# Optimization experiments

Hardware: AMD Instinct MI355X
Metric: run time of the kernel (lower is better)

## Reference

```python
import jax, jax.numpy as jnp
import numpy as np

DIN = 256
HID = 512

def setup_inputs() -> dict:
    key = jax.random.key(0)
    ks = jax.random.split(key, 9)
    s_in = 1.0 / np.sqrt(DIN)
    s_h = 1.0 / np.sqrt(HID)
    h = jax.random.normal(ks[0], (32, 1024, DIN), dtype=jnp.float32)
    Wv = jax.random.uniform(ks[1], (HID, DIN), jnp.float32, -s_in, s_in)
    bv = jax.random.uniform(ks[2], (HID,), jnp.float32, -s_in, s_in)
    Wk = jax.random.uniform(ks[3], (HID, DIN), jnp.float32, -s_in, s_in)
    bk = jax.random.uniform(ks[4], (HID,), jnp.float32, -s_in, s_in)
    Wq = jax.random.uniform(ks[5], (HID, DIN), jnp.float32, -s_in, s_in)
    bq = jax.random.uniform(ks[6], (HID,), jnp.float32, -s_in, s_in)
    Wo = jax.random.uniform(ks[7], (DIN, HID), jnp.float32, -s_h, s_h)
    bo = jax.random.uniform(ks[8], (DIN,), jnp.float32, -s_h, s_h)
    return {"h": h, "Wv": Wv, "bv": bv, "Wk": Wk, "bk": bk, "Wq": Wq, "bq": bq, "Wo": Wo, "bo": bo}

def reference(h, Wv, bv, Wk, bk, Wq, bq, Wo, bo):
    # relu-activated Q/K/V projections: [B, N, HID]
    v = jax.nn.relu(jnp.einsum('bnd,hd->bnh', h, Wv) + bv)
    q = jax.nn.relu(jnp.einsum('bnd,hd->bnh', h, Wq) + bq)
    k = jax.nn.relu(jnp.einsum('bnd,hd->bnh', h, Wk) + bk)
    # unscaled attention: [B, N, N]
    att = jax.nn.softmax(jnp.einsum('bnh,bmh->bnm', q, k), axis=2)
    out = jnp.einsum('bnm,bmh->bnh', att, v)          # [B, N, HID]
    out = jax.nn.relu(jnp.einsum('bnh,dh->bnd', out, Wo) + bo)  # [B, N, DIN]
    return out
```

## Files before the change

### kernel.cpp

```cpp
#include <hip/hip_runtime.h>
#include <cstdint>
#include <cstddef>

#define NB    32
#define SEQ   1024
#define DIN   256
#define HID   512
#define MTOT  32768

typedef _Float16 half_t;
typedef _Float16 half8  __attribute__((ext_vector_type(8)));
typedef _Float16 half4v __attribute__((ext_vector_type(4)));
typedef float    f32x4  __attribute__((ext_vector_type(4)));

typedef __attribute__((address_space(1))) const void* gas_ptr;
typedef __attribute__((address_space(3))) void*       las_ptr;

__global__ void cvt_kernel(const float* __restrict__ src, half_t* __restrict__ dst, int n4) {
    int i = blockIdx.x * blockDim.x + threadIdx.x;
    if (i < n4) {
        f32x4 v = ((const f32x4*)src)[i];
        half4v h;
        h[0] = (half_t)v[0]; h[1] = (half_t)v[1]; h[2] = (half_t)v[2]; h[3] = (half_t)v[3];
        ((half4v*)dst)[i] = h;
    }
}

__global__ void cvt4_kernel(const float* __restrict__ s0, const float* __restrict__ s1,
                            const float* __restrict__ s2, const float* __restrict__ s3,
                            half_t* __restrict__ d0, half_t* __restrict__ d1,
                            half_t* __restrict__ d2, half_t* __restrict__ d3, int n4) {
    int y = blockIdx.y;
    const float* s = y == 0 ? s0 : y == 1 ? s1 : y == 2 ? s2 : s3;
    half_t*      d = y == 0 ? d0 : y == 1 ? d1 : y == 2 ? d2 : d3;
    int i = blockIdx.x * blockDim.x + threadIdx.x;
    if (i < n4) {
        f32x4 v = ((const f32x4*)s)[i];
        half4v h;
        h[0] = (half_t)v[0]; h[1] = (half_t)v[1]; h[2] = (half_t)v[2]; h[3] = (half_t)v[3];
        ((half4v*)d)[i] = h;
    }
}

__global__ void pack_bias(const float* __restrict__ bv, const float* __restrict__ bk,
                          const float* __restrict__ bq, float* __restrict__ dst) {
    int t = threadIdx.x;
    if (t < HID) {
        dst[t]         = bv[t];
        dst[HID + t]   = bk[t];
        dst[2*HID + t] = bq[t];
    }
}

template<int MODE>
__global__ __launch_bounds__(256, 2) void gemm_k(
    const half_t* __restrict__ A, long lda, long a_bs,
    const half_t* __restrict__ Bw, long ldb, long b_bs,
    void* __restrict__ Out, long ldo, long o_bs,
    const float* __restrict__ bias,
    int Kdim, half_t* __restrict__ out2)
{
    __shared__ alignas(16) half_t As[128 * 32];
    __shared__ alignas(16) half_t Bs[128 * 32];

    const int t    = threadIdx.x;
    const int lane = t & 63;
    const int wave = t >> 6;
    const int wm   = wave >> 1;
    const int wn   = wave & 1;
    const int lanen = lane & 15;
    const int quad  = lane >> 4;
    const int z     = blockIdx.z;
    const long m0 = (long)blockIdx.x * 128;
    const long n0 = (long)blockIdx.y * 128;

    const half_t* Ab = A  + (long)z * a_bs;
    const half_t* Bb = Bw + (long)z * b_bs;

    f32x4 acc[4][4];
#pragma unroll
    for (int i = 0; i < 4; i++)
#pragma unroll
        for (int j = 0; j < 4; j++)
            acc[i][j] = f32x4{0.f, 0.f, 0.f, 0.f};

    const int c0 = t, c1 = t + 256;
    const int r0 = c0 >> 2, kc0 = c0 & 3;
    const int r1 = c1 >> 2, kc1 = c1 & 3;

    const half_t* gA0 = Ab + (m0 + r0) * lda + kc0 * 8;
    const half_t* gA1 = Ab + (m0 + r1) * lda + kc1 * 8;
    const half_t* gB0 = Bb + (n0 + r0) * ldb + kc0 * 8;
    const half_t* gB1 = Bb + (n0 + r1) * ldb + kc1 * 8;
    half_t* lA0 = &As[c0 * 8];
    half_t* lA1 = &As[c1 * 8];
    half_t* lB0 = &Bs[c0 * 8];
    half_t* lB1 = &Bs[c1 * 8];

    int aoff[4], boff[4];
#pragma unroll
    for (int i = 0; i < 4; i++) aoff[i] = (wm * 64 + i * 16 + lanen) * 32 + quad * 8;
#pragma unroll
    for (int j = 0; j < 4; j++) boff[j] = (wn * 64 + j * 16 + lanen) * 32 + quad * 8;

    for (int k0 = 0; k0 < Kdim; k0 += 32) {
        __builtin_amdgcn_global_load_lds((gas_ptr)(gA0 + k0), (las_ptr)lA0, 16, 0, 0);
        __builtin_amdgcn_global_load_lds((gas_ptr)(gA1 + k0), (las_ptr)lA1, 16, 0, 0);
        __builtin_amdgcn_global_load_lds((gas_ptr)(gB0 + k0), (las_ptr)lB0, 16, 0, 0);
        __builtin_amdgcn_global_load_lds((gas_ptr)(gB1 + k0), (las_ptr)lB1, 16, 0, 0);
        __syncthreads();

        half8 af[4], bf[4];
#pragma unroll
        for (int i = 0; i < 4; i++) af[i] = *(const half8*)&As[aoff[i]];
#pragma unroll
        for (int j = 0; j < 4; j++) bf[j] = *(const half8*)&Bs[boff[j]];
#pragma unroll
        for (int i = 0; i < 4; i++)
#pragma unroll
            for (int j = 0; j < 4; j++)
                acc[i][j] = __builtin_amdgcn_mfma_f32_16x16x32_f16(af[i], bf[j], acc[i][j], 0, 0, 0);
        __syncthreads();
    }

#pragma unroll
    for (int i = 0; i < 4; i++) {
        long mrow = m0 + wm * 64 + i * 16 + quad * 4;
#pragma unroll
        for (int j = 0; j < 4; j++) {
            long gn = n0 + wn * 64 + j * 16 + lanen;
            f32x4 v = acc[i][j];
            if (MODE == 0) {
                float bb = bias[z * HID + gn];
                half_t h0 = (half_t)fmaxf(v[0] + bb, 0.f);
                half_t h1 = (half_t)fmaxf(v[1] + bb, 0.f);
                half_t h2 = (half_t)fmaxf(v[2] + bb, 0.f);
                half_t h3 = (half_t)fmaxf(v[3] + bb, 0.f);
                if (z == 0) {
                    long bidx = mrow >> 10;
                    long pos  = mrow & 1023;
                    half4v pk; pk[0] = h0; pk[1] = h1; pk[2] = h2; pk[3] = h3;
                    *(half4v*)(out2 + ((bidx * HID + gn) << 10) + pos) = pk;
                } else {
                    half_t* o = (half_t*)Out + (long)(z - 1) * o_bs;
                    o[(mrow + 0) * ldo + gn] = h0;
                    o[(mrow + 1) * ldo + gn] = h1;
                    o[(mrow + 2) * ldo + gn] = h2;
                    o[(mrow + 3) * ldo + gn] = h3;
                }
            } else {
                float* o = (float*)Out;
                float bb = bias[gn];
#pragma unroll
                for (int r = 0; r < 4; r++) o[(mrow + r) * ldo + gn] = fmaxf(v[r] + bb, 0.f);
            }
        }
    }
}

__global__ __launch_bounds__(256, 2) void se_k(
    const half_t* __restrict__ Q, const half_t* __restrict__ K,
    half_t* __restrict__ E, float* __restrict__ Mstat, float* __restrict__ Lstat)
{
    __shared__ alignas(16) half_t As[128 * 32];
    __shared__ alignas(16) half_t Bs[256 * 32];

    const int t    = threadIdx.x;
    const int lane = t & 63;
    const int wave = t >> 6;
    const int wm   = wave >> 1;
    const int wn   = wave & 1;
    const int lanen = lane & 15;
    const int quad  = lane >> 4;
    const int z     = blockIdx.z;
    const long m0 = (long)blockIdx.x * 128;
    const long n0 = (long)blockIdx.y * 256;

    const half_t* Ab = Q + (long)z * SEQ * HID;
    const half_t* Bb = K + (long)z * SEQ * HID;

    f32x4 acc[4][8];
#pragma unroll
    for (int i = 0; i < 4; i++)
#pragma unroll
        for (int j = 0; j < 8; j++)
            acc[i][j] = f32x4{0.f, 0.f, 0.f, 0.f};

    const half_t* gA[2]; half_t* lA[2];
    const half_t* gB[4]; half_t* lB[4];
#pragma unroll
    for (int s = 0; s < 2; s++) {
        int c = t + 256 * s;
        gA[s] = Ab + (m0 + (c >> 2)) * HID + (c & 3) * 8;
        lA[s] = &As[c * 8];
    }
#pragma unroll
    for (int s = 0; s < 4; s++) {
        int c = t + 256 * s;
        gB[s] = Bb + (n0 + (c >> 2)) * HID + (c & 3) * 8;
        lB[s] = &Bs[c * 8];
    }

    int aoff[4], boff[8];
#pragma unroll
    for (int i = 0; i < 4; i++) aoff[i] = (wm * 64 + i * 16 + lanen) * 32 + quad * 8;
#pragma unroll
    for (int j = 0; j < 8; j++) boff[j] = (wn * 128 + j * 16 + lanen) * 32 + quad * 8;

    for (int k0 = 0; k0 < HID; k0 += 32) {
#pragma unroll
        for (int s = 0; s < 2; s++)
            __builtin_amdgcn_global_load_lds((gas_ptr)(gA[s] + k0), (las_ptr)lA[s], 16, 0, 0);
#pragma unroll
        for (int s = 0; s < 4; s++)
            __builtin_amdgcn_global_load_lds((gas_ptr)(gB[s] + k0), (las_ptr)lB[s], 16, 0, 0);
        __syncthreads();

        half8 af[4], bf[8];
#pragma unroll
        for (int i = 0; i < 4; i++) af[i] = *(const half8*)&As[aoff[i]];
#pragma unroll
        for (int j = 0; j < 8; j++) bf[j] = *(const half8*)&Bs[boff[j]];
#pragma unroll
        for (int i = 0; i < 4; i++)
#pragma unroll
            for (int j = 0; j < 8; j++)
                acc[i][j] = __builtin_amdgcn_mfma_f32_16x16x32_f16(af[i], bf[j], acc[i][j], 0, 0, 0);
        __syncthreads();
    }

    float mf[4][4];
#pragma unroll
    for (int i = 0; i < 4; i++)
#pragma unroll
        for (int r = 0; r < 4; r++) {
            float v = acc[i][0][r];
#pragma unroll
            for (int j = 1; j < 8; j++) v = fmaxf(v, acc[i][j][r]);
#pragma unroll
            for (int off = 8; off > 0; off >>= 1)
                v = fmaxf(v, __shfl_xor(v, off, 64));
            mf[i][r] = v;
        }

    half_t* Eb = E + (long)z * SEQ * SEQ;
    float rs[4][4];
#pragma unroll
    for (int i = 0; i < 4; i++)
#pragma unroll
        for (int r = 0; r < 4; r++) rs[i][r] = 0.f;
#pragma unroll
    for (int i = 0; i < 4; i++) {
        long mrow = m0 + wm * 64 + i * 16 + quad * 4;
#pragma unroll
        for (int j = 0; j < 8; j++) {
            long gn = n0 + wn * 128 + j * 16 + lanen;
#pragma unroll
            for (int r = 0; r < 4; r++) {
                float e = __expf(acc[i][j][r] - mf[i][r]);
                rs[i][r] += e;
                Eb[(mrow + r) * SEQ + gn] = (half_t)e;
            }
        }
    }
#pragma unroll
    for (int i = 0; i < 4; i++)
#pragma unroll
        for (int r = 0; r < 4; r++) {
            float v = rs[i][r];
#pragma unroll
            for (int off = 8; off > 0; off >>= 1)
                v += __shfl_xor(v, off, 64);
            rs[i][r] = v;
        }

    if (lanen == 0) {
        long base = ((long)z * 8 + blockIdx.y * 2 + wn) * SEQ + m0 + wm * 64;
#pragma unroll
        for (int i = 0; i < 4; i++)
#pragma unroll
            for (int r = 0; r < 4; r++) {
                Mstat[base + i * 16 + quad * 4 + r] = mf[i][r];
                Lstat[base + i * 16 + quad * 4 + r] = rs[i][r];
            }
    }
}

__global__ __launch_bounds__(256, 2) void pv_k(
    const half_t* __restrict__ E, const half_t* __restrict__ vT,
    const float* __restrict__ Mstat, const float* __restrict__ Lstat,
    half_t* __restrict__ O16)
{
    __shared__ alignas(16) half_t As[128 * 32];
    __shared__ alignas(16) half_t Bs[256 * 32];
    __shared__ float scaleS[8][128];
    __shared__ float invS[128];

    const int t    = threadIdx.x;
    const int lane = t & 63;
    const int wave = t >> 6;
    const int wm   = wave >> 1;
    const int wn   = wave & 1;
    const int lanen = lane & 15;
    const int quad  = lane >> 4;
    const int z     = blockIdx.z;
    const long m0 = (long)blockIdx.x * 128;
    const long h0 = (long)blockIdx.y * 256;

    if (t < 128) {
        float mv[8];
        float M = -1e30f;
#pragma unroll
        for (int kb = 0; kb < 8; kb++) {
            mv[kb] = Mstat[((long)z * 8 + kb) * SEQ + m0 + t];
            M = fmaxf(M, mv[kb]);
        }
        float ls = 0.f;
#pragma unroll
        for (int kb = 0; kb < 8; kb++) {
            float sc = __expf(mv[kb] - M);
            scaleS[kb][t] = sc;
            ls += Lstat[((long)z * 8 + kb) * SEQ + m0 + t] * sc;
        }
        invS[t] = 1.f / ls;
    }
    __syncthreads();

    const half_t* Ab = E  + (long)z * SEQ * SEQ;
    const half_t* Bb = vT + (long)z * HID * SEQ;

    f32x4 acc[4][8];
#pragma unroll
    for (int i = 0; i < 4; i++)
#pragma unroll
        for (int j = 0; j < 8; j++)
            acc[i][j] = f32x4{0.f, 0.f, 0.f, 0.f};

    const half_t* gA[2]; half_t* lA[2];
    const half_t* gB[4]; half_t* lB[4];
#pragma unroll
    for (int s = 0; s < 2; s++) {
        int c = t + 256 * s;
        gA[s] = Ab + (m0 + (c >> 2)) * SEQ + (c & 3) * 8;
        lA[s] = &As[c * 8];
    }
#pragma unroll
    for (int s = 0; s < 4; s++) {
        int c = t + 256 * s;
        gB[s] = Bb + (h0 + (c >> 2)) * SEQ + (c & 3) * 8;
        lB[s] = &Bs[c * 8];
    }

    int aoff[4], boff[8];
#pragma unroll
    for (int i = 0; i < 4; i++) aoff[i] = (wm * 64 + i * 16 + lanen) * 32 + quad * 8;
#pragma unroll
    for (int j = 0; j < 8; j++) boff[j] = (wn * 128 + j * 16 + lanen) * 32 + quad * 8;

    for (int k0 = 0; k0 < SEQ; k0 += 32) {
#pragma unroll
        for (int s = 0; s < 2; s++)
            __builtin_amdgcn_global_load_lds((gas_ptr)(gA[s] + k0), (las_ptr)lA[s], 16, 0, 0);
#pragma unroll
        for (int s = 0; s < 4; s++)
            __builtin_amdgcn_global_load_lds((gas_ptr)(gB[s] + k0), (las_ptr)lB[s], 16, 0, 0);
        __syncthreads();

        const int kb = k0 >> 7;
        half8 af[4], bf[8];
#pragma unroll
        for (int i = 0; i < 4; i++) {
            af[i] = *(const half8*)&As[aoff[i]];
            half_t sh = (half_t)scaleS[kb][wm * 64 + i * 16 + lanen];
            af[i] *= sh;
        }
#pragma unroll
        for (int j = 0; j < 8; j++) bf[j] = *(const half8*)&Bs[boff[j]];
#pragma unroll
        for (int i = 0; i < 4; i++)
#pragma unroll
            for (int j = 0; j < 8; j++)
                acc[i][j] = __builtin_amdgcn_mfma_f32_16x16x32_f16(af[i], bf[j], acc[i][j], 0, 0, 0);
        __syncthreads();
    }

    half_t* o = O16 + (long)z * SEQ * HID;
#pragma unroll
    for (int i = 0; i < 4; i++) {
        long mrow = m0 + wm * 64 + i * 16 + quad * 4;
        int rl = wm * 64 + i * 16 + quad * 4;
#pragma unroll
        for (int j = 0; j < 8; j++) {
            long gn = h0 + wn * 128 + j * 16 + lanen;
#pragma unroll
            for (int r = 0; r < 4; r++)
                o[(mrow + r) * HID + gn] = (half_t)(acc[i][j][r] * invS[rl + r]);
        }
    }
}

extern "C" void kernel_launch(void* const* d_in, const int* in_sizes, int n_in,
                              void* d_out, int out_size, void* d_ws, size_t ws_size,
                              hipStream_t stream) {
    const float* h  = (const float*)d_in[0];
    const float* Wv = (const float*)d_in[1];
    const float* bv = (const float*)d_in[2];
    const float* Wk = (const float*)d_in[3];
    const float* bk = (const float*)d_in[4];
    const float* Wq = (const float*)d_in[5];
    const float* bq = (const float*)d_in[6];
    const float* Wo = (const float*)d_in[7];
    const float* bo = (const float*)d_in[8];

    uint8_t* ws = (uint8_t*)d_ws;
    size_t off = 0;
    auto alloc = [&](size_t bytes) { size_t o = off; off += (bytes + 255) & ~(size_t)255; return o; };

    half_t* W16   = (half_t*)(ws + alloc((size_t)3 * HID * DIN * 2));
    half_t* Wo16  = (half_t*)(ws + alloc((size_t)DIN * HID * 2));
    float*  biasq = (float*)(ws + alloc((size_t)3 * HID * 4));
    half_t* k16   = (half_t*)(ws + alloc((size_t)MTOT * HID * 2));
    half_t* q16   = (half_t*)(ws + alloc((size_t)MTOT * HID * 2));
    half_t* vT    = (half_t*)(ws + alloc((size_t)MTOT * HID * 2));
    size_t h16_off = alloc((size_t)MTOT * DIN * 2);
    half_t* h16   = (half_t*)(ws + h16_off);
    half_t* O16 = q16;

    size_t s_avail = ws_size > h16_off ? ws_size - h16_off : 0;
    size_t per_batch = (size_t)SEQ * SEQ * 2 + 2 * 8 * SEQ * 4;
    int GB = (int)(s_avail / per_batch);
    if (GB < 1)  GB = 1;
    if (GB > NB) GB = NB;
    half_t* Ebuf  = (half_t*)(ws + h16_off);
    float*  Mstat = (float*)(ws + h16_off + (size_t)GB * SEQ * SEQ * 2);
    float*  Lstat = Mstat + (size_t)GB * 8 * SEQ;

    cvt_kernel<<<dim3((MTOT * DIN / 4 + 255) / 256), 256, 0, stream>>>(h, h16, MTOT * DIN / 4);
    cvt4_kernel<<<dim3((HID * DIN / 4 + 255) / 256, 4), 256, 0, stream>>>(
        Wv, Wk, Wq, Wo, W16, W16 + HID * DIN, W16 + 2 * HID * DIN, Wo16, HID * DIN / 4);
    pack_bias<<<dim3(1), 512, 0, stream>>>(bv, bk, bq, biasq);

    gemm_k<0><<<dim3(MTOT / 128, HID / 128, 3), 256, 0, stream>>>(
        h16, DIN, 0,
        W16, DIN, (long)HID * DIN,
        (void*)k16, HID, (long)MTOT * HID,
        biasq, DIN, vT);

    for (int g0 = 0; g0 < NB; g0 += GB) {
        int gb = NB - g0 < GB ? NB - g0 : GB;
        se_k<<<dim3(SEQ / 128, SEQ / 256, gb), 256, 0, stream>>>(
            q16 + (size_t)g0 * SEQ * HID,
            k16 + (size_t)g0 * SEQ * HID,
            Ebuf, Mstat, Lstat);
        pv_k<<<dim3(SEQ / 128, HID / 256, gb), 256, 0, stream>>>(
            Ebuf, vT + (size_t)g0 * HID * SEQ,
            Mstat, Lstat,
            O16 + (size_t)g0 * SEQ * HID);
    }

    gemm_k<3><<<dim3(MTOT / 128, DIN / 128, 1), 256, 0, stream>>>(
        O16, HID, 0,
        Wo16, HID, 0,
        d_out, DIN, 0,
        bo, HID, nullptr);

    (void)in_sizes; (void)n_in; (void)out_size;
}
```

Before: 290.8 us.

## Swap MFMA operands for vectorized stores, merge conversion kernels, cap batch group

Three prep kernels (h, weight and bias conversion) are merged into one launch. The MFMA operands are swapped in the score, PV and output GEMMs so each lane holds four consecutive columns. That lets the epilogues write half4/float4 vectors instead of scattered scalars, and shrinks the softmax row reductions to two cross-lane shuffles. The batch group size is capped at 16, which may add an extra se/pv launch round but keeps the E buffer smaller and more cache-friendly.

```diff
diff --git a/kernel.cpp b/kernel.cpp
--- a/kernel.cpp
+++ b/kernel.cpp
@@ -16,39 +16,35 @@
 typedef __attribute__((address_space(1))) const void* gas_ptr;
 typedef __attribute__((address_space(3))) void*       las_ptr;
 
-__global__ void cvt_kernel(const float* __restrict__ src, half_t* __restrict__ dst, int n4) {
-    int i = blockIdx.x * blockDim.x + threadIdx.x;
-    if (i < n4) {
-        f32x4 v = ((const f32x4*)src)[i];
-        half4v h;
-        h[0] = (half_t)v[0]; h[1] = (half_t)v[1]; h[2] = (half_t)v[2]; h[3] = (half_t)v[3];
-        ((half4v*)dst)[i] = h;
-    }
-}
-
-__global__ void cvt4_kernel(const float* __restrict__ s0, const float* __restrict__ s1,
-                            const float* __restrict__ s2, const float* __restrict__ s3,
-                            half_t* __restrict__ d0, half_t* __restrict__ d1,
-                            half_t* __restrict__ d2, half_t* __restrict__ d3, int n4) {
-    int y = blockIdx.y;
-    const float* s = y == 0 ? s0 : y == 1 ? s1 : y == 2 ? s2 : s3;
-    half_t*      d = y == 0 ? d0 : y == 1 ? d1 : y == 2 ? d2 : d3;
-    int i = blockIdx.x * blockDim.x + threadIdx.x;
-    if (i < n4) {
+__global__ void cvt_all(const float* __restrict__ h,
+                        const float* __restrict__ Wv, const float* __restrict__ Wk,
+                        const float* __restrict__ Wq, const float* __restrict__ Wo,
+                        const float* __restrict__ bv, const float* __restrict__ bk,
+                        const float* __restrict__ bq,
+                        half_t* __restrict__ h16, half_t* __restrict__ W16,
+                        half_t* __restrict__ Wo16, float* __restrict__ biasq) {
+    int b = blockIdx.x;
+    if (b < 8192) {
+        int i = b * 256 + threadIdx.x;
+        f32x4 v = ((const f32x4*)h)[i];
+        half4v o;
+        o[0] = (half_t)v[0]; o[1] = (half_t)v[1]; o[2] = (half_t)v[2]; o[3] = (half_t)v[3];
+        ((half4v*)h16)[i] = o;
+    } else if (b < 8704) {
+        int w = (b - 8192) >> 7;
+        int i = ((b - 8192) & 127) * 256 + threadIdx.x;
+        const float* s = w == 0 ? Wv : w == 1 ? Wk : w == 2 ? Wq : Wo;
+        half_t*      d = w < 3 ? W16 + (size_t)w * HID * DIN : Wo16;
         f32x4 v = ((const f32x4*)s)[i];
-        half4v h;
-        h[0] = (half_t)v[0]; h[1] = (half_t)v[1]; h[2] = (half_t)v[2]; h[3] = (half_t)v[3];
-        ((half4v*)d)[i] = h;
-    }
-}
-
-__global__ void pack_bias(const float* __restrict__ bv, const float* __restrict__ bk,
-                          const float* __restrict__ bq, float* __restrict__ dst) {
-    int t = threadIdx.x;
-    if (t < HID) {
-        dst[t]         = bv[t];
-        dst[HID + t]   = bk[t];
-        dst[2*HID + t] = bq[t];
+        half4v o;
+        o[0] = (half_t)v[0]; o[1] = (half_t)v[1]; o[2] = (half_t)v[2]; o[3] = (half_t)v[3];
+        ((half4v*)d)[i] = o;
+    } else {
+        for (int i = threadIdx.x; i < HID; i += 256) {
+            biasq[i]           = bv[i];
+            biasq[HID + i]     = bk[i];
+            biasq[2 * HID + i] = bq[i];
+        }
     }
 }
 
@@ -118,19 +114,23 @@
 #pragma unroll
         for (int i = 0; i < 4; i++)
 #pragma unroll
-            for (int j = 0; j < 4; j++)
-                acc[i][j] = __builtin_amdgcn_mfma_f32_16x16x32_f16(af[i], bf[j], acc[i][j], 0, 0, 0);
-        __syncthreads();
-    }
-
-#pragma unroll
-    for (int i = 0; i < 4; i++) {
-        long mrow = m0 + wm * 64 + i * 16 + quad * 4;
-#pragma unroll
-        for (int j = 0; j < 4; j++) {
-            long gn = n0 + wn * 64 + j * 16 + lanen;
-            f32x4 v = acc[i][j];
-            if (MODE == 0) {
+            for (int j = 0; j < 4; j++) {
+                if (MODE == 3)
+                    acc[i][j] = __builtin_amdgcn_mfma_f32_16x16x32_f16(bf[j], af[i], acc[i][j], 0, 0, 0);
+                else
+                    acc[i][j] = __builtin_amdgcn_mfma_f32_16x16x32_f16(af[i], bf[j], acc[i][j], 0, 0, 0);
+            }
+        __syncthreads();
+    }
+
+    if (MODE == 0) {
+#pragma unroll
+        for (int i = 0; i < 4; i++) {
+            long mrow = m0 + wm * 64 + i * 16 + quad * 4;
+#pragma unroll
+            for (int j = 0; j < 4; j++) {
+                long gn = n0 + wn * 64 + j * 16 + lanen;
+                f32x4 v = acc[i][j];
                 float bb = bias[z * HID + gn];
                 half_t h0 = (half_t)fmaxf(v[0] + bb, 0.f);
                 half_t h1 = (half_t)fmaxf(v[1] + bb, 0.f);
@@ -148,11 +148,22 @@
                     o[(mrow + 2) * ldo + gn] = h2;
                     o[(mrow + 3) * ldo + gn] = h3;
                 }
-            } else {
-                float* o = (float*)Out;
-                float bb = bias[gn];
-#pragma unroll
-                for (int r = 0; r < 4; r++) o[(mrow + r) * ldo + gn] = fmaxf(v[r] + bb, 0.f);
+            }
+        }
+    } else {
+        float* o = (float*)Out;
+#pragma unroll
+        for (int i = 0; i < 4; i++) {
+            long mrow = m0 + wm * 64 + i * 16 + lanen;
+#pragma unroll
+            for (int j = 0; j < 4; j++) {
+                long gn = n0 + wn * 64 + j * 16 + quad * 4;
+                f32x4 bb = *(const f32x4*)&bias[gn];
+                f32x4 v = acc[i][j];
+                f32x4 ov;
+#pragma unroll
+                for (int r = 0; r < 4; r++) ov[r] = fmaxf(v[r] + bb[r], 0.f);
+                *(f32x4*)&o[mrow * ldo + gn] = ov;
             }
         }
     }
@@ -225,64 +236,56 @@
         for (int i = 0; i < 4; i++)
 #pragma unroll
             for (int j = 0; j < 8; j++)
-                acc[i][j] = __builtin_amdgcn_mfma_f32_16x16x32_f16(af[i], bf[j], acc[i][j], 0, 0, 0);
-        __syncthreads();
-    }
-
-    float mf[4][4];
-#pragma unroll
-    for (int i = 0; i < 4; i++)
-#pragma unroll
-        for (int r = 0; r < 4; r++) {
-            float v = acc[i][0][r];
-#pragma unroll
-            for (int j = 1; j < 8; j++) v = fmaxf(v, acc[i][j][r]);
-#pragma unroll
-            for (int off = 8; off > 0; off >>= 1)
-                v = fmaxf(v, __shfl_xor(v, off, 64));
-            mf[i][r] = v;
-        }
+                acc[i][j] = __builtin_amdgcn_mfma_f32_16x16x32_f16(bf[j], af[i], acc[i][j], 0, 0, 0);
+        __syncthreads();
+    }
+
+    float mf[4];
+#pragma unroll
+    for (int i = 0; i < 4; i++) {
+        float v = acc[i][0][0];
+#pragma unroll
+        for (int j = 0; j < 8; j++)
+#pragma unroll
+            for (int r = 0; r < 4; r++) v = fmaxf(v, acc[i][j][r]);
+        v = fmaxf(v, __shfl_xor(v, 16, 64));
+        v = fmaxf(v, __shfl_xor(v, 32, 64));
+        mf[i] = v;
+    }
 
     half_t* Eb = E + (long)z * SEQ * SEQ;
-    float rs[4][4];
-#pragma unroll
-    for (int i = 0; i < 4; i++)
-#pragma unroll
-        for (int r = 0; r < 4; r++) rs[i][r] = 0.f;
+    float rs[4] = {0.f, 0.f, 0.f, 0.f};
 #pragma unroll
     for (int i = 0; i < 4; i++) {
-        long mrow = m0 + wm * 64 + i * 16 + quad * 4;
+        long qrow = m0 + wm * 64 + i * 16 + lanen;
 #pragma unroll
         for (int j = 0; j < 8; j++) {
-            long gn = n0 + wn * 128 + j * 16 + lanen;
+            long gn = n0 + wn * 128 + j * 16 + quad * 4;
+            half4v hv;
 #pragma unroll
             for (int r = 0; r < 4; r++) {
-                float e = __expf(acc[i][j][r] - mf[i][r]);
-                rs[i][r] += e;
-                Eb[(mrow + r) * SEQ + gn] = (half_t)e;
+                float e = __expf(acc[i][j][r] - mf[i]);
+                rs[i] += e;
+                hv[r] = (half_t)e;
             }
-        }
-    }
-#pragma unroll
-    for (int i = 0; i < 4; i++)
-#pragma unroll
-        for (int r = 0; r < 4; r++) {
-            float v = rs[i][r];
-#pragma unroll
-            for (int off = 8; off > 0; off >>= 1)
-                v += __shfl_xor(v, off, 64);
-            rs[i][r] = v;
-        }
-
-    if (lanen == 0) {
+            *(half4v*)(Eb + qrow * SEQ + gn) = hv;
+        }
+    }
+#pragma unroll
+    for (int i = 0; i < 4; i++) {
+        float v = rs[i];
+        v += __shfl_xor(v, 16, 64);
+        v += __shfl_xor(v, 32, 64);
+        rs[i] = v;
+    }
+
+    if (quad == 0) {
         long base = ((long)z * 8 + blockIdx.y * 2 + wn) * SEQ + m0 + wm * 64;
 #pragma unroll
-        for (int i = 0; i < 4; i++)
-#pragma unroll
-            for (int r = 0; r < 4; r++) {
-                Mstat[base + i * 16 + quad * 4 + r] = mf[i][r];
-                Lstat[base + i * 16 + quad * 4 + r] = rs[i][r];
-            }
+        for (int i = 0; i < 4; i++) {
+            Mstat[base + i * 16 + lanen] = mf[i];
+            Lstat[base + i * 16 + lanen] = rs[i];
+        }
     }
 }
 
@@ -380,21 +383,23 @@
         for (int i = 0; i < 4; i++)
 #pragma unroll
             for (int j = 0; j < 8; j++)
-                acc[i][j] = __builtin_amdgcn_mfma_f32_16x16x32_f16(af[i], bf[j], acc[i][j], 0, 0, 0);
+                acc[i][j] = __builtin_amdgcn_mfma_f32_16x16x32_f16(bf[j], af[i], acc[i][j], 0, 0, 0);
         __syncthreads();
     }
 
     half_t* o = O16 + (long)z * SEQ * HID;
 #pragma unroll
     for (int i = 0; i < 4; i++) {
-        long mrow = m0 + wm * 64 + i * 16 + quad * 4;
-        int rl = wm * 64 + i * 16 + quad * 4;
+        int qrl = wm * 64 + i * 16 + lanen;
+        long qrow = m0 + qrl;
+        float inv = invS[qrl];
 #pragma unroll
         for (int j = 0; j < 8; j++) {
-            long gn = h0 + wn * 128 + j * 16 + lanen;
-#pragma unroll
-            for (int r = 0; r < 4; r++)
-                o[(mrow + r) * HID + gn] = (half_t)(acc[i][j][r] * invS[rl + r]);
+            long gn = h0 + wn * 128 + j * 16 + quad * 4;
+            half4v hv;
+#pragma unroll
+            for (int r = 0; r < 4; r++) hv[r] = (half_t)(acc[i][j][r] * inv);
+            *(half4v*)(o + qrow * HID + gn) = hv;
         }
     }
 }
@@ -429,16 +434,14 @@
     size_t s_avail = ws_size > h16_off ? ws_size - h16_off : 0;
     size_t per_batch = (size_t)SEQ * SEQ * 2 + 2 * 8 * SEQ * 4;
     int GB = (int)(s_avail / per_batch);
+    if (GB > 16) GB = 16;
     if (GB < 1)  GB = 1;
-    if (GB > NB) GB = NB;
     half_t* Ebuf  = (half_t*)(ws + h16_off);
     float*  Mstat = (float*)(ws + h16_off + (size_t)GB * SEQ * SEQ * 2);
     float*  Lstat = Mstat + (size_t)GB * 8 * SEQ;
 
-    cvt_kernel<<<dim3((MTOT * DIN / 4 + 255) / 256), 256, 0, stream>>>(h, h16, MTOT * DIN / 4);
-    cvt4_kernel<<<dim3((HID * DIN / 4 + 255) / 256, 4), 256, 0, stream>>>(
-        Wv, Wk, Wq, Wo, W16, W16 + HID * DIN, W16 + 2 * HID * DIN, Wo16, HID * DIN / 4);
-    pack_bias<<<dim3(1), 512, 0, stream>>>(bv, bk, bq, biasq);
+    cvt_all<<<dim3(8705), 256, 0, stream>>>(h, Wv, Wk, Wq, Wo, bv, bk, bq,
+                                            h16, W16, Wo16, biasq);
 
     gemm_k<0><<<dim3(MTOT / 128, HID / 128, 3), 256, 0, stream>>>(
         h16, DIN, 0,
```

Measured after the change: 313.8 us. +7.9%, slower.
